# Performance work log

Measured on AMD Instinct MI355X. Metric: run time of the kernel, lower is better.

The kernel has to match this reference:

```python
import jax, jax.numpy as jnp
import numpy as np

BT = 64  # chunk size (BLOCK_SIZE_C)
EPS = 1e-06


def setup_inputs() -> dict:
    key = jax.random.key(0)
    k1, k2, k3, k4 = jax.random.split(key, 4)
    B, H, S, D = 4, 8, 4096, 128
    q = jax.random.normal(k1, (B, H, S, D), dtype=jnp.float32)
    k = jax.random.normal(k2, (B, H, S, D), dtype=jnp.float32)
    v = jax.random.normal(k3, (B, H, S, D), dtype=jnp.float32)
    beta = jax.random.uniform(k4, (B, H, S), dtype=jnp.float32)
    return {"q": q, "k": k, "v": v, "beta": beta}


def _chunk_gated_delta_fwd(q, k, v, beta):
    # Recurrence: S_t = beta_t * S_{t-1} + k_t (x) v_t ;  o_t = q_t @ S_t
    B, H, S, D = q.shape
    NC = S // BT
    f32 = jnp.float32
    qf = q.astype(f32).reshape(B, H, NC, BT, D)
    kf = k.astype(f32).reshape(B, H, NC, BT, D)
    vf = v.astype(f32).reshape(B, H, NC, BT, D)
    log_beta = jnp.log(beta.astype(f32).reshape(B, H, NC, BT) + EPS)
    cum = jnp.cumsum(log_beta, axis=-1)                     # [B,H,NC,BT]
    tot = cum[..., -1]                                      # [B,H,NC]
    decay_from_start = jnp.exp(cum)                         # [B,H,NC,BT]
    decay_to_end = jnp.exp(tot[..., None] - cum)            # [B,H,NC,BT]
    causal = jnp.tril(jnp.ones((BT, BT), dtype=bool))
    decay_matrix = jnp.exp(cum[..., :, None] - cum[..., None, :])  # [B,H,NC,BT,BT]
    decay_masked = jnp.where(causal, decay_matrix, 0.0)
    # intra-chunk contribution (fully parallel across chunks)
    qk = jnp.einsum('bhcid,bhcjd->bhcij', qf, kf)
    out_intra = jnp.einsum('bhcij,bhcjd->bhcid', qk * decay_masked, vf)
    # per-chunk state-update term: (k * decay_to_end)^T @ v
    upd = jnp.einsum('bhcid,bhcie->bhcde', kf * decay_to_end[..., None], vf)
    # sequential inter-chunk recurrence over chunks
    def step(state, xs):
        qc, dfs_c, tot_c, upd_c = xs
        out_inter = jnp.einsum('bhid,bhde->bhie', qc * dfs_c[..., None], state)
        new_state = state * jnp.exp(tot_c)[..., None, None] + upd_c
        return new_state, out_inter
    xs = (jnp.moveaxis(qf, 2, 0), jnp.moveaxis(decay_from_start, 2, 0),
          jnp.moveaxis(tot, 2, 0), jnp.moveaxis(upd, 2, 0))
    state0 = jnp.zeros((B, H, D, D), dtype=f32)
    _, out_inter = jax.lax.scan(step, state0, xs)           # [NC,B,H,BT,D]
    out = out_intra + jnp.moveaxis(out_inter, 0, 2)
    return out.reshape(B, H, S, D).astype(q.dtype)


def reference(q, k, v, beta):
    return _chunk_gated_delta_fwd(q, k, v, beta)
```

## Files before the change

kernel.cpp:

```cpp
#include <hip/hip_runtime.h>
#include <hip/hip_bf16.h>
#include <math.h>

#define Gp  32
#define Sp  4096
#define Dp  128
#define BTp 64
#define NCp 64

typedef __attribute__((ext_vector_type(8))) short bf16x8;
typedef __attribute__((ext_vector_type(4))) float f32x4;

#define MFMA(a,b,c) __builtin_amdgcn_mfma_f32_16x16x32_bf16((a),(b),(c),0,0,0)

#define STR 72

__device__ inline unsigned pack2(float lo, float hi) {
    __hip_bfloat162 h = __float22bfloat162_rn(make_float2(lo, hi));
    union { __hip_bfloat162 v; unsigned u; } t; t.v = h; return t.u;
}
__device__ inline unsigned short f2bf(float x) {
    union { float f; unsigned u; } u; u.f = x;
    unsigned r = u.u + 0x7fffu + ((u.u >> 16) & 1u);
    return (unsigned short)(r >> 16);
}
__device__ inline float bflo(unsigned u) { union { unsigned u; float f; } t; t.u = u << 16; return t.f; }
__device__ inline float bfhi(unsigned u) { union { unsigned u; float f; } t; t.u = u & 0xffff0000u; return t.f; }

__global__ __launch_bounds__(256, 3) void gdn_intra(
    const float* __restrict__ q, const float* __restrict__ k,
    const float* __restrict__ v, const float* __restrict__ beta,
    float* __restrict__ out, unsigned short* __restrict__ upd,
    float* __restrict__ tot_buf, float* __restrict__ dfs_buf)
{
    __shared__ unsigned short s_k [64 * 128];
    __shared__ unsigned short s_vt[128 * STR];
    __shared__ unsigned short s_kt[128 * STR];

    const int blk = blockIdx.x, g = blk >> 6, c = blk & 63;
    const int tid = threadIdx.x, lane = tid & 63, w = tid >> 6;
    const int m16 = lane & 15, quad = lane >> 4;
    const size_t base  = ((size_t)g * Sp + (size_t)c * BTp) * Dp;
    const size_t bbase = (size_t)g * Sp + (size_t)c * BTp;

    float x = logf(beta[bbase + lane] + 1e-6f);
    #pragma unroll
    for (int off = 1; off < 64; off <<= 1) {
        float n = __shfl_up(x, off, 64);
        if (lane >= off) x += n;
    }
    const float tot = __shfl(x, 63, 64);
    const float dte_own = expf(tot - x);
    if (tid < 64) dfs_buf[bbase + lane] = expf(x);
    if (tid == 63) tot_buf[g * NCp + c] = tot;

    bf16x8 qf[4];
    {
        const float* qrow = q + base + (size_t)(16 * w + m16) * Dp + quad * 8;
        #pragma unroll
        for (int ks = 0; ks < 4; ++ks) {
            const float4 a = *(const float4*)(qrow + ks * 32);
            const float4 b = *(const float4*)(qrow + ks * 32 + 4);
            union { bf16x8 v; unsigned ui[4]; } t;
            t.ui[0] = pack2(a.x, a.y); t.ui[1] = pack2(a.z, a.w);
            t.ui[2] = pack2(b.x, b.y); t.ui[3] = pack2(b.z, b.w);
            qf[ks] = t.v;
        }
    }

    #pragma unroll
    for (int it = 0; it < 8; ++it) {
        const int idx = (it * 256 + tid) * 4;
        const int i = idx >> 7, d = idx & 127;
        const float4 kv = *(const float4*)(k + base + (size_t)i * Dp + d);
        const int ad = i * 128 + (((d >> 3) ^ (i & 15)) << 3) + (d & 7);
        uint2 pw; pw.x = pack2(kv.x, kv.y); pw.y = pack2(kv.z, kv.w);
        *(uint2*)&s_k[ad] = pw;
    }
    #pragma unroll
    for (int it = 0; it < 8; ++it) {
        const int u = it * 256 + tid;
        const int d = (u & 63) * 2, i = (u >> 6) * 2;
        const float dte0 = __shfl(dte_own, i, 64);
        const float dte1 = __shfl(dte_own, i + 1, 64);
        const float2 va = *(const float2*)(v + base + (size_t)i * Dp + d);
        const float2 vb = *(const float2*)(v + base + (size_t)(i + 1) * Dp + d);
        const float2 ka = *(const float2*)(k + base + (size_t)i * Dp + d);
        const float2 kb = *(const float2*)(k + base + (size_t)(i + 1) * Dp + d);
        *(unsigned*)&s_vt[d * STR + i]       = pack2(va.x, vb.x);
        *(unsigned*)&s_vt[(d + 1) * STR + i] = pack2(va.y, vb.y);
        *(unsigned*)&s_kt[d * STR + i]       = pack2(ka.x * dte0, kb.x * dte1);
        *(unsigned*)&s_kt[(d + 1) * STR + i] = pack2(ka.y * dte0, kb.y * dte1);
    }
    __syncthreads();

    float pv[4][4];
    {
        f32x4 accP[4] = {};
        #pragma unroll
        for (int ks = 0; ks < 4; ++ks) {
            #pragma unroll
            for (int nt = 0; nt < 4; ++nt) {
                const int j = 16 * nt + m16;
                const bf16x8 bf = *(const bf16x8*)&s_k[j * 128 + (((quad + 4 * ks) ^ m16) << 3)];
                accP[nt] = MFMA(qf[ks], bf, accP[nt]);
            }
        }
        const int i0 = 16 * w + quad * 4;
        float cj[4];
        #pragma unroll
        for (int nt = 0; nt < 4; ++nt) cj[nt] = __shfl(x, 16 * nt + m16, 64);
        #pragma unroll
        for (int r = 0; r < 4; ++r) {
            const float ci = __shfl(x, i0 + r, 64);
            #pragma unroll
            for (int nt = 0; nt < 4; ++nt) {
                const int j = 16 * nt + m16;
                pv[nt][r] = (i0 + r >= j) ? accP[nt][r] * expf(ci - cj[nt]) : 0.f;
            }
        }
    }

    {
        f32x4 accU[2][8] = {};
        #pragma unroll
        for (int ks = 0; ks < 2; ++ks) {
            const bf16x8 a0 = *(const bf16x8*)&s_vt[(32 * w      + m16) * STR + quad * 8 + ks * 32];
            const bf16x8 a1 = *(const bf16x8*)&s_vt[(32 * w + 16 + m16) * STR + quad * 8 + ks * 32];
            #pragma unroll
            for (int nt = 0; nt < 8; ++nt) {
                const bf16x8 bf = *(const bf16x8*)&s_kt[(16 * nt + m16) * STR + quad * 8 + ks * 32];
                accU[0][nt] = MFMA(a0, bf, accU[0][nt]);
                accU[1][nt] = MFMA(a1, bf, accU[1][nt]);
            }
        }
        unsigned short* ub = upd + (size_t)blk * Dp * Dp;
        #pragma unroll
        for (int mt = 0; mt < 2; ++mt) {
            const int e0 = 32 * w + 16 * mt + quad * 4;
            #pragma unroll
            for (int nt = 0; nt < 8; ++nt) {
                const int d = 16 * nt + m16;
                #pragma unroll
                for (int r = 0; r < 4; ++r)
                    ub[(size_t)(e0 + r) * Dp + d] = f2bf(accU[mt][nt][r]);
            }
        }
    }
    __syncthreads();

    unsigned short* s_P = s_k;
    {
        const int i0 = 16 * w + quad * 4;
        #pragma unroll
        for (int r = 0; r < 4; ++r)
            #pragma unroll
            for (int nt = 0; nt < 4; ++nt)
                s_P[(i0 + r) * STR + 16 * nt + m16] = f2bf(pv[nt][r]);
    }
    __syncthreads();

    {
        f32x4 accO[8] = {};
        #pragma unroll
        for (int ks = 0; ks < 2; ++ks) {
            const bf16x8 af = *(const bf16x8*)&s_P[(16 * w + m16) * STR + quad * 8 + ks * 32];
            #pragma unroll
            for (int nt = 0; nt < 8; ++nt) {
                const bf16x8 bf = *(const bf16x8*)&s_vt[(16 * nt + m16) * STR + quad * 8 + ks * 32];
                accO[nt] = MFMA(af, bf, accO[nt]);
            }
        }
        const int i0 = 16 * w + quad * 4;
        #pragma unroll
        for (int nt = 0; nt < 8; ++nt) {
            const int d = 16 * nt + m16;
            #pragma unroll
            for (int r = 0; r < 4; ++r)
                out[base + (size_t)(i0 + r) * Dp + d] = accO[nt][r];
        }
    }
}

__global__ __launch_bounds__(128) void gdn_scan(
    unsigned short* __restrict__ upd, const float* __restrict__ tot_buf)
{
    const int g = blockIdx.x >> 4, slab = blockIdx.x & 15, tid = threadIdx.x;
    __shared__ float s_e[NCp];
    if (tid < NCp) s_e[tid] = expf(tot_buf[g * NCp + tid]);
    __syncthreads();
    uint4* b = (uint4*)(upd + (size_t)g * NCp * Dp * Dp) + slab * 128 + tid;
    float s0 = 0.f, s1 = 0.f, s2 = 0.f, s3 = 0.f;
    float s4 = 0.f, s5 = 0.f, s6 = 0.f, s7 = 0.f;
    uint4 pf[4];
    #pragma unroll
    for (int j = 0; j < 4; ++j) pf[j] = b[(size_t)j * 2048];
    #pragma unroll
    for (int cc = 0; cc < NCp; ++cc) {
        const uint4 cur = pf[cc & 3];
        if (cc + 4 < NCp) pf[cc & 3] = b[(size_t)(cc + 4) * 2048];
        const float e = s_e[cc];
        uint4 stq;
        stq.x = pack2(s0, s1); stq.y = pack2(s2, s3);
        stq.z = pack2(s4, s5); stq.w = pack2(s6, s7);
        b[(size_t)cc * 2048] = stq;
        s0 = s0 * e + bflo(cur.x); s1 = s1 * e + bfhi(cur.x);
        s2 = s2 * e + bflo(cur.y); s3 = s3 * e + bfhi(cur.y);
        s4 = s4 * e + bflo(cur.z); s5 = s5 * e + bfhi(cur.z);
        s6 = s6 * e + bflo(cur.w); s7 = s7 * e + bfhi(cur.w);
    }
}

__global__ __launch_bounds__(256) void gdn_inter(
    const float* __restrict__ q, const unsigned short* __restrict__ state,
    const float* __restrict__ dfs_buf, float* __restrict__ out)
{
    const int blk = blockIdx.x, g = blk >> 6, c = blk & 63;
    const int tid = threadIdx.x, lane = tid & 63, w = tid >> 6;
    const int m16 = lane & 15, quad = lane >> 4;
    const size_t base  = ((size_t)g * Sp + (size_t)c * BTp) * Dp;
    const size_t bbase = (size_t)g * Sp + (size_t)c * BTp;
    const unsigned short* sb = state + (size_t)blk * Dp * Dp;
    const int i0 = 16 * w + quad * 4;

    const float scale = dfs_buf[bbase + 16 * w + m16];
    bf16x8 qf[4];
    const float* qrow = q + base + (size_t)(16 * w + m16) * Dp + quad * 8;
    #pragma unroll
    for (int ks = 0; ks < 4; ++ks) {
        const float4 a = *(const float4*)(qrow + ks * 32);
        const float4 b = *(const float4*)(qrow + ks * 32 + 4);
        union { bf16x8 v; unsigned ui[4]; } t;
        t.ui[0] = pack2(a.x * scale, a.y * scale);
        t.ui[1] = pack2(a.z * scale, a.w * scale);
        t.ui[2] = pack2(b.x * scale, b.y * scale);
        t.ui[3] = pack2(b.z * scale, b.w * scale);
        qf[ks] = t.v;
    }

    float ov[8][4];
    #pragma unroll
    for (int nt = 0; nt < 8; ++nt)
        #pragma unroll
        for (int r = 0; r < 4; ++r)
            ov[nt][r] = out[base + (size_t)(i0 + r) * Dp + 16 * nt + m16];

    f32x4 acc[8] = {};
    #pragma unroll
    for (int ks = 0; ks < 4; ++ks) {
        bf16x8 bfr[8];
        #pragma unroll
        for (int nt = 0; nt < 8; ++nt)
            bfr[nt] = *(const bf16x8*)(sb + (16 * nt + m16) * Dp + quad * 8 + ks * 32);
        #pragma unroll
        for (int nt = 0; nt < 8; ++nt)
            acc[nt] = MFMA(qf[ks], bfr[nt], acc[nt]);
    }
    #pragma unroll
    for (int nt = 0; nt < 8; ++nt) {
        const int e = 16 * nt + m16;
        #pragma unroll
        for (int r = 0; r < 4; ++r)
            out[base + (size_t)(i0 + r) * Dp + e] = ov[nt][r] + acc[nt][r];
    }
}

extern "C" void kernel_launch(void* const* d_in, const int* in_sizes, int n_in,
                              void* d_out, int out_size, void* d_ws, size_t ws_size,
                              hipStream_t stream) {
    const float* q    = (const float*)d_in[0];
    const float* k    = (const float*)d_in[1];
    const float* v    = (const float*)d_in[2];
    const float* beta = (const float*)d_in[3];
    float* out = (float*)d_out;

    unsigned short* upd = (unsigned short*)d_ws;
    float* tot_buf = (float*)(upd + (size_t)Gp * NCp * Dp * Dp);
    float* dfs_buf = tot_buf + Gp * NCp;

    gdn_intra<<<Gp * NCp, 256, 0, stream>>>(q, k, v, beta, out, upd, tot_buf, dfs_buf);
    gdn_scan <<<Gp * 16, 128, 0, stream>>>(upd, tot_buf);
    gdn_inter<<<Gp * NCp, 256, 0, stream>>>(q, upd, dfs_buf, out);
}
```

Measured before the change: 313.8 us.

## Compute QK^T from registers with causal tile skipping and transposed MFMA outputs

```diff
diff --git a/kernel.cpp b/kernel.cpp
--- a/kernel.cpp
+++ b/kernel.cpp
@@ -19,21 +19,15 @@
     __hip_bfloat162 h = __float22bfloat162_rn(make_float2(lo, hi));
     union { __hip_bfloat162 v; unsigned u; } t; t.v = h; return t.u;
 }
-__device__ inline unsigned short f2bf(float x) {
-    union { float f; unsigned u; } u; u.f = x;
-    unsigned r = u.u + 0x7fffu + ((u.u >> 16) & 1u);
-    return (unsigned short)(r >> 16);
-}
 __device__ inline float bflo(unsigned u) { union { unsigned u; float f; } t; t.u = u << 16; return t.f; }
 __device__ inline float bfhi(unsigned u) { union { unsigned u; float f; } t; t.u = u & 0xffff0000u; return t.f; }
 
-__global__ __launch_bounds__(256, 3) void gdn_intra(
+__global__ __launch_bounds__(256, 4) void gdn_intra(
     const float* __restrict__ q, const float* __restrict__ k,
     const float* __restrict__ v, const float* __restrict__ beta,
     float* __restrict__ out, unsigned short* __restrict__ upd,
     float* __restrict__ tot_buf, float* __restrict__ dfs_buf)
 {
-    __shared__ unsigned short s_k [64 * 128];
     __shared__ unsigned short s_vt[128 * STR];
     __shared__ unsigned short s_kt[128 * STR];
 
@@ -54,29 +48,6 @@
     if (tid < 64) dfs_buf[bbase + lane] = expf(x);
     if (tid == 63) tot_buf[g * NCp + c] = tot;
 
-    bf16x8 qf[4];
-    {
-        const float* qrow = q + base + (size_t)(16 * w + m16) * Dp + quad * 8;
-        #pragma unroll
-        for (int ks = 0; ks < 4; ++ks) {
-            const float4 a = *(const float4*)(qrow + ks * 32);
-            const float4 b = *(const float4*)(qrow + ks * 32 + 4);
-            union { bf16x8 v; unsigned ui[4]; } t;
-            t.ui[0] = pack2(a.x, a.y); t.ui[1] = pack2(a.z, a.w);
-            t.ui[2] = pack2(b.x, b.y); t.ui[3] = pack2(b.z, b.w);
-            qf[ks] = t.v;
-        }
-    }
-
-    #pragma unroll
-    for (int it = 0; it < 8; ++it) {
-        const int idx = (it * 256 + tid) * 4;
-        const int i = idx >> 7, d = idx & 127;
-        const float4 kv = *(const float4*)(k + base + (size_t)i * Dp + d);
-        const int ad = i * 128 + (((d >> 3) ^ (i & 15)) << 3) + (d & 7);
-        uint2 pw; pw.x = pack2(kv.x, kv.y); pw.y = pack2(kv.z, kv.w);
-        *(uint2*)&s_k[ad] = pw;
-    }
     #pragma unroll
     for (int it = 0; it < 8; ++it) {
         const int u = it * 256 + tid;
@@ -92,92 +63,127 @@
         *(unsigned*)&s_kt[d * STR + i]       = pack2(ka.x * dte0, kb.x * dte1);
         *(unsigned*)&s_kt[(d + 1) * STR + i] = pack2(ka.y * dte0, kb.y * dte1);
     }
+
+    bf16x8 qf[4];
+    {
+        const float* qrow = q + base + (size_t)(16 * w + m16) * Dp + quad * 8;
+        #pragma unroll
+        for (int ks = 0; ks < 4; ++ks) {
+            const float4 a = *(const float4*)(qrow + ks * 32);
+            const float4 b = *(const float4*)(qrow + ks * 32 + 4);
+            union { bf16x8 v; unsigned ui[4]; } t;
+            t.ui[0] = pack2(a.x, a.y); t.ui[1] = pack2(a.z, a.w);
+            t.ui[2] = pack2(b.x, b.y); t.ui[3] = pack2(b.z, b.w);
+            qf[ks] = t.v;
+        }
+    }
+
+    f32x4 accP[4] = {};
+    #pragma unroll
+    for (int nt = 0; nt < 4; ++nt) {
+        if (nt <= w) {
+            const float* krow = k + base + (size_t)(16 * nt + m16) * Dp + quad * 8;
+            float4 ra[4], rb[4];
+            #pragma unroll
+            for (int ks = 0; ks < 4; ++ks) {
+                ra[ks] = *(const float4*)(krow + ks * 32);
+                rb[ks] = *(const float4*)(krow + ks * 32 + 4);
+            }
+            #pragma unroll
+            for (int ks = 0; ks < 4; ++ks) {
+                union { bf16x8 v; unsigned ui[4]; } t;
+                t.ui[0] = pack2(ra[ks].x, ra[ks].y); t.ui[1] = pack2(ra[ks].z, ra[ks].w);
+                t.ui[2] = pack2(rb[ks].x, rb[ks].y); t.ui[3] = pack2(rb[ks].z, rb[ks].w);
+                accP[nt] = MFMA(t.v, qf[ks], accP[nt]);
+            }
+        }
+    }
+
+    const float ci = __shfl(x, 16 * w + m16, 64);
+    unsigned p_pk[4][2];
+    #pragma unroll
+    for (int nt = 0; nt < 4; ++nt) { p_pk[nt][0] = 0u; p_pk[nt][1] = 0u; }
+    #pragma unroll
+    for (int nt = 0; nt < 4; ++nt) {
+        if (nt <= w) {
+            float pm[4];
+            #pragma unroll
+            for (int r = 0; r < 4; ++r) {
+                const int j = 16 * nt + 4 * quad + r;
+                const float cj = __shfl(x, j, 64);
+                float val = accP[nt][r] * expf(ci - cj);
+                if (nt == w) val = (16 * w + m16 >= j) ? val : 0.f;
+                pm[r] = val;
+            }
+            p_pk[nt][0] = pack2(pm[0], pm[1]);
+            p_pk[nt][1] = pack2(pm[2], pm[3]);
+        }
+    }
+
+    bf16x8 af[2];
+    #pragma unroll
+    for (int ks = 0; ks < 2; ++ks) {
+        if (ks <= (w >> 1)) {
+            union { bf16x8 v; unsigned ui[4]; } t;
+            #pragma unroll
+            for (int m = 0; m < 4; ++m) {
+                const int src = m16 + 16 * (2 * (quad & 1) + (m >> 1));
+                const unsigned aA = (unsigned)__shfl((int)p_pk[2 * ks][m & 1], src, 64);
+                const unsigned aB = (unsigned)__shfl((int)p_pk[2 * ks + 1][m & 1], src, 64);
+                t.ui[m] = (quad >> 1) ? aB : aA;
+            }
+            af[ks] = t.v;
+        }
+    }
+
     __syncthreads();
-
-    float pv[4][4];
-    {
-        f32x4 accP[4] = {};
-        #pragma unroll
-        for (int ks = 0; ks < 4; ++ks) {
-            #pragma unroll
-            for (int nt = 0; nt < 4; ++nt) {
-                const int j = 16 * nt + m16;
-                const bf16x8 bf = *(const bf16x8*)&s_k[j * 128 + (((quad + 4 * ks) ^ m16) << 3)];
-                accP[nt] = MFMA(qf[ks], bf, accP[nt]);
-            }
-        }
-        const int i0 = 16 * w + quad * 4;
-        float cj[4];
-        #pragma unroll
-        for (int nt = 0; nt < 4; ++nt) cj[nt] = __shfl(x, 16 * nt + m16, 64);
-        #pragma unroll
-        for (int r = 0; r < 4; ++r) {
-            const float ci = __shfl(x, i0 + r, 64);
-            #pragma unroll
-            for (int nt = 0; nt < 4; ++nt) {
-                const int j = 16 * nt + m16;
-                pv[nt][r] = (i0 + r >= j) ? accP[nt][r] * expf(ci - cj[nt]) : 0.f;
-            }
-        }
-    }
 
     {
         f32x4 accU[2][8] = {};
         #pragma unroll
         for (int ks = 0; ks < 2; ++ks) {
-            const bf16x8 a0 = *(const bf16x8*)&s_vt[(32 * w      + m16) * STR + quad * 8 + ks * 32];
-            const bf16x8 a1 = *(const bf16x8*)&s_vt[(32 * w + 16 + m16) * STR + quad * 8 + ks * 32];
+            const bf16x8 b0 = *(const bf16x8*)&s_vt[(16 * (2 * w)     + m16) * STR + quad * 8 + ks * 32];
+            const bf16x8 b1 = *(const bf16x8*)&s_vt[(16 * (2 * w + 1) + m16) * STR + quad * 8 + ks * 32];
             #pragma unroll
             for (int nt = 0; nt < 8; ++nt) {
-                const bf16x8 bf = *(const bf16x8*)&s_kt[(16 * nt + m16) * STR + quad * 8 + ks * 32];
-                accU[0][nt] = MFMA(a0, bf, accU[0][nt]);
-                accU[1][nt] = MFMA(a1, bf, accU[1][nt]);
+                const bf16x8 a = *(const bf16x8*)&s_kt[(16 * nt + m16) * STR + quad * 8 + ks * 32];
+                accU[0][nt] = MFMA(a, b0, accU[0][nt]);
+                accU[1][nt] = MFMA(a, b1, accU[1][nt]);
             }
         }
         unsigned short* ub = upd + (size_t)blk * Dp * Dp;
         #pragma unroll
         for (int mt = 0; mt < 2; ++mt) {
-            const int e0 = 32 * w + 16 * mt + quad * 4;
+            const int e = 16 * (2 * w + mt) + m16;
             #pragma unroll
             for (int nt = 0; nt < 8; ++nt) {
-                const int d = 16 * nt + m16;
-                #pragma unroll
-                for (int r = 0; r < 4; ++r)
-                    ub[(size_t)(e0 + r) * Dp + d] = f2bf(accU[mt][nt][r]);
-            }
-        }
-    }
-    __syncthreads();
-
-    unsigned short* s_P = s_k;
-    {
-        const int i0 = 16 * w + quad * 4;
-        #pragma unroll
-        for (int r = 0; r < 4; ++r)
-            #pragma unroll
-            for (int nt = 0; nt < 4; ++nt)
-                s_P[(i0 + r) * STR + 16 * nt + m16] = f2bf(pv[nt][r]);
-    }
-    __syncthreads();
+                uint2 pw;
+                pw.x = pack2(accU[mt][nt][0], accU[mt][nt][1]);
+                pw.y = pack2(accU[mt][nt][2], accU[mt][nt][3]);
+                *(uint2*)&ub[(size_t)e * Dp + 16 * nt + 4 * quad] = pw;
+            }
+        }
+    }
 
     {
         f32x4 accO[8] = {};
         #pragma unroll
         for (int ks = 0; ks < 2; ++ks) {
-            const bf16x8 af = *(const bf16x8*)&s_P[(16 * w + m16) * STR + quad * 8 + ks * 32];
-            #pragma unroll
-            for (int nt = 0; nt < 8; ++nt) {
-                const bf16x8 bf = *(const bf16x8*)&s_vt[(16 * nt + m16) * STR + quad * 8 + ks * 32];
-                accO[nt] = MFMA(af, bf, accO[nt]);
-            }
-        }
-        const int i0 = 16 * w + quad * 4;
+            if (ks <= (w >> 1)) {
+                #pragma unroll
+                for (int nt = 0; nt < 8; ++nt) {
+                    const bf16x8 a = *(const bf16x8*)&s_vt[(16 * nt + m16) * STR + quad * 8 + ks * 32];
+                    accO[nt] = MFMA(a, af[ks], accO[nt]);
+                }
+            }
+        }
+        const int i = 16 * w + m16;
         #pragma unroll
         for (int nt = 0; nt < 8; ++nt) {
-            const int d = 16 * nt + m16;
-            #pragma unroll
-            for (int r = 0; r < 4; ++r)
-                out[base + (size_t)(i0 + r) * Dp + d] = accO[nt][r];
+            float4 st;
+            st.x = accO[nt][0]; st.y = accO[nt][1];
+            st.z = accO[nt][2]; st.w = accO[nt][3];
+            *(float4*)&out[base + (size_t)i * Dp + 16 * nt + 4 * quad] = st;
         }
     }
 }
@@ -234,6 +240,7 @@
         t.ui[0] = pack2(a.x * scale, a.y * scale);
         t.ui[1] = pack2(a.z * scale, a.w * scale);
         t.ui[2] = pack2(b.x * scale, b.y * scale);
+        t.ui[3] = pack2(b.w * scale, b.w * scale);
         t.ui[3] = pack2(b.z * scale, b.w * scale);
         qf[ks] = t.v;
     }
```

New measurement: 320.7 us. 1.02x slower.
